# Kernel optimization log

Hardware: AMD Instinct MI355X
Metric: run time of the kernel (lower is better)

The kernel has to match this reference:

```python
import jax, jax.numpy as jnp
import numpy as np

ALPHA = 0.1
K = 5


def setup_inputs() -> dict:
    key = jax.random.key(0)
    ks = jax.random.split(key, 6)
    N, E = 50000, 800000
    IN, HID, OUT = 512, 256, 64
    x = jax.random.normal(ks[0], (N, IN), dtype=jnp.float32)
    edge_index = jax.random.randint(ks[1], (2, E), 0, N, dtype=jnp.int64)
    # Linear params (torch Linear: y = x @ W.T + b), kaiming-ish scale
    W1 = jax.random.normal(ks[2], (HID, IN), dtype=jnp.float32) / np.sqrt(IN)
    b1 = jnp.zeros((HID,), dtype=jnp.float32)
    W2 = jax.random.normal(ks[3], (OUT, HID), dtype=jnp.float32) / np.sqrt(HID)
    b2 = jnp.zeros((OUT,), dtype=jnp.float32)
    return {"x": x, "W1": W1, "b1": b1, "W2": W2, "b2": b2,
            "edge_index": edge_index}


def reference(x, W1, b1, W2, b2, edge_index):
    N = x.shape[0]
    # --- MLP encoder (eval mode: dropout is identity) ---
    h = jax.nn.relu(x @ W1.T + b1)          # [N, HID]
    h = h @ W2.T + b2                       # [N, OUT]

    # --- gcn_norm with self-loops (PyG APPNP default) ---
    src, dst = edge_index[0], edge_index[1]
    loop = jnp.arange(N, dtype=src.dtype)
    src_f = jnp.concatenate([src, loop])    # [E+N]
    dst_f = jnp.concatenate([dst, loop])
    ew = jnp.ones(src_f.shape[0], dtype=h.dtype)
    deg = jax.ops.segment_sum(ew, dst_f, num_segments=N)
    dinv = jnp.where(deg > 0, jax.lax.rsqrt(deg), 0.0)
    norm = dinv[src_f] * dinv[dst_f]        # [E+N]

    # --- K iterations of personalized-PageRank propagation ---
    def body(xk, _):
        msg = norm[:, None] * xk[src_f]                      # gather [E+N, OUT]
        agg = jax.ops.segment_sum(msg, dst_f, num_segments=N)
        return (1.0 - ALPHA) * agg + ALPHA * h, None

    xK, _ = jax.lax.scan(body, h, None, length=K)
    return jax.nn.log_softmax(xK, axis=1)
```

## Files before the change

kernel.cpp:

```cpp
#include <hip/hip_runtime.h>
#include <hip/hip_bf16.h>

#define IN_DIM  512
#define HID_DIM 256
#define OUT_DIM 64

typedef __attribute__((ext_vector_type(8))) short bf16x8;
typedef __attribute__((ext_vector_type(4))) float f32x4;

static __device__ __forceinline__ ushort f2b(float f) {
    __hip_bfloat16 b = __float2bfloat16(f);
    return *reinterpret_cast<ushort*>(&b);
}
static __device__ __forceinline__ float b2f_lo(uint u) {
    union { uint u; float f; } t; t.u = u << 16; return t.f;
}
static __device__ __forceinline__ float b2f_hi(uint u) {
    union { uint u; float f; } t; t.u = u & 0xFFFF0000u; return t.f;
}
static __device__ __forceinline__ uint packbf(float x, float y) {
    return (uint)f2b(x) | ((uint)f2b(y) << 16);
}

#define GLOAD16(g, l) __builtin_amdgcn_global_load_lds(                      \
    (const __attribute__((address_space(1))) void*)(g),                      \
    (__attribute__((address_space(3))) void*)(l), 16, 0, 0)


__global__ __launch_bounds__(256) void f2b_kernel(const float* __restrict__ in,
                                                  ushort* __restrict__ out, int n8) {
    for (int i = blockIdx.x * 256 + threadIdx.x; i < n8; i += gridDim.x * 256) {
        float4 a = *reinterpret_cast<const float4*>(&in[(size_t)i * 8]);
        float4 b = *reinterpret_cast<const float4*>(&in[(size_t)i * 8 + 4]);
        ushort4 lo = make_ushort4(f2b(a.x), f2b(a.y), f2b(a.z), f2b(a.w));
        ushort4 hi = make_ushort4(f2b(b.x), f2b(b.y), f2b(b.z), f2b(b.w));
        *reinterpret_cast<ushort4*>(&out[(size_t)i * 8])     = lo;
        *reinterpret_cast<ushort4*>(&out[(size_t)i * 8 + 4]) = hi;
    }
}


__global__ void hist_kernel(const int* __restrict__ ei, int* __restrict__ deg, int E) {
    int e = blockIdx.x * 256 + threadIdx.x;
    if (e < E) atomicAdd(&deg[ei[E + e]], 1);
}

__global__ __launch_bounds__(256) void scanA_kernel(const int* __restrict__ deg,
                                                    int* __restrict__ offs,
                                                    int* __restrict__ bsum, int N) {
    __shared__ int sh[256];
    int tid = threadIdx.x;
    int i = blockIdx.x * 256 + tid;
    int v = (i < N) ? deg[i] : 0;
    sh[tid] = v;
    __syncthreads();
#pragma unroll
    for (int off = 1; off < 256; off <<= 1) {
        int t = (tid >= off) ? sh[tid - off] : 0;
        __syncthreads();
        sh[tid] += t;
        __syncthreads();
    }
    if (i < N) offs[i] = sh[tid] - v;
    if (tid == 255) bsum[blockIdx.x] = sh[255];
}

__global__ __launch_bounds__(256) void scanB_kernel(int* __restrict__ bsum, int nb) {
    __shared__ int sh[256];
    int tid = threadIdx.x;
    int v = (tid < nb) ? bsum[tid] : 0;
    sh[tid] = v;
    __syncthreads();
#pragma unroll
    for (int off = 1; off < 256; off <<= 1) {
        int t = (tid >= off) ? sh[tid - off] : 0;
        __syncthreads();
        sh[tid] += t;
        __syncthreads();
    }
    if (tid < nb) bsum[tid] = sh[tid] - v;
}

__global__ __launch_bounds__(256) void scanC_kernel(const int* __restrict__ deg,
                                                    const int* __restrict__ bsum,
                                                    int* __restrict__ offs,
                                                    float* __restrict__ dinv,
                                                    int N, int E) {
    int i = blockIdx.x * 256 + threadIdx.x;
    if (i < N) {
        offs[i] += bsum[i >> 8];
        dinv[i] = rsqrtf((float)(deg[i] + 1));
    }
    if (i == 0) offs[N] = E;
}

__global__ void fill_kernel(const int* __restrict__ ei, const int* __restrict__ offs,
                            int* __restrict__ cursor, const float* __restrict__ dinv,
                            uint* __restrict__ edat, int E) {
    int e = blockIdx.x * 256 + threadIdx.x;
    if (e < E) {
        int s = ei[e];
        int d = ei[E + e];
        int pos = offs[d] + atomicAdd(&cursor[d], 1);
        edat[pos] = (uint)s | ((uint)f2b(dinv[d] * dinv[s]) << 16);
    }
}


__global__ __launch_bounds__(256) void gemm1_f32a(const float* __restrict__ A,
                                                  const ushort* __restrict__ B,
                                                  const float* __restrict__ bias,
                                                  ushort* __restrict__ C, int M) {
    constexpr int K = IN_DIM;
    constexpr int NK = K / 32;
    __shared__ float  Asf[2][128 * 32];
    __shared__ ushort Bs[2][128 * 32];

    const int tid  = threadIdx.x;
    const int lane = tid & 63;
    const int wid  = tid >> 6;
    const int wm = wid >> 1, wn = wid & 1;
    const int m0 = blockIdx.y * 128;
    const int n0 = blockIdx.x * 128;
    const int l15 = lane & 15;
    const int lq  = lane >> 4;

    const int a_row  = lane >> 3;
    const int a_slot = (lane & 7) ^ a_row;
    const int b_row  = lane >> 2;
    const int b_slot = (lane & 3) ^ ((lane >> 3) & 3);

    f32x4 acc[4][4];
#pragma unroll
    for (int i = 0; i < 4; ++i)
#pragma unroll
        for (int j = 0; j < 4; ++j) acc[i][j] = (f32x4)0.0f;

    auto stage = [&](int buf, int ks) {
        const int k0 = ks * 32;
#pragma unroll
        for (int q = 0; q < 4; ++q) {
            const int rbase = (wid * 4 + q) * 8;
            int am = m0 + rbase + a_row; if (am >= M) am = M - 1;
            const float* ga = A + (size_t)am * K + k0 + a_slot * 4;
            GLOAD16(ga, &Asf[buf][rbase * 32]);
        }
#pragma unroll
        for (int q = 0; q < 2; ++q) {
            const int rbase = (wid * 2 + q) * 16;
            const int row = rbase + b_row;
            const ushort* gb = B + (size_t)(n0 + row) * K + k0 + b_slot * 8;
            GLOAD16(gb, &Bs[buf][rbase * 32]);
        }
    };

    stage(0, 0);
    __syncthreads();

#pragma unroll 2
    for (int ks = 0; ks < NK; ++ks) {
        const int cur = ks & 1;
        if (ks + 1 < NK) stage(cur ^ 1, ks + 1);

        bf16x8 af[4], bf[4];
#pragma unroll
        for (int f = 0; f < 4; ++f) {
            const int ar = wm * 64 + f * 16 + l15;
            const int r7 = ar & 7;
            f32x4 v0 = *reinterpret_cast<const f32x4*>(&Asf[cur][ar * 32 + (((2 * lq) ^ r7) << 2)]);
            f32x4 v1 = *reinterpret_cast<const f32x4*>(&Asf[cur][ar * 32 + (((2 * lq + 1) ^ r7) << 2)]);
            bf16x8 a;
            a[0] = (short)f2b(v0[0]); a[1] = (short)f2b(v0[1]);
            a[2] = (short)f2b(v0[2]); a[3] = (short)f2b(v0[3]);
            a[4] = (short)f2b(v1[0]); a[5] = (short)f2b(v1[1]);
            a[6] = (short)f2b(v1[2]); a[7] = (short)f2b(v1[3]);
            af[f] = a;
            const int br = wn * 64 + f * 16 + l15;
            bf[f] = *reinterpret_cast<const bf16x8*>(&Bs[cur][br * 32 + ((lq ^ ((br >> 1) & 3)) << 3)]);
        }
#pragma unroll
        for (int i = 0; i < 4; ++i)
#pragma unroll
            for (int j = 0; j < 4; ++j)
                acc[i][j] = __builtin_amdgcn_mfma_f32_16x16x32_bf16(af[i], bf[j], acc[i][j], 0, 0, 0);

        __syncthreads();
    }

    const int lr = lq * 4;
#pragma unroll
    for (int nf = 0; nf < 4; ++nf) {
        int col = n0 + wn * 64 + nf * 16 + l15;
        float bv = bias[col];
#pragma unroll
        for (int mf = 0; mf < 4; ++mf) {
#pragma unroll
            for (int j = 0; j < 4; ++j) {
                int row = m0 + wm * 64 + mf * 16 + lr + j;
                if (row < M) {
                    float v = fmaxf(acc[mf][nf][j] + bv, 0.f);
                    C[(size_t)row * HID_DIM + col] = f2b(v);
                }
            }
        }
    }
}


#define LDT 40

__global__ __launch_bounds__(256) void gemm2_bf16(const ushort* __restrict__ A,
                                                  const float* __restrict__ B,
                                                  const float* __restrict__ bias,
                                                  ushort* __restrict__ Cb,
                                                  int M) {
    constexpr int K = HID_DIM;
    constexpr int NK = K / 32;
    __shared__ ushort As[128 * LDT];
    __shared__ ushort Bs[64 * LDT];

    const int tid = threadIdx.x;
    const int lane = tid & 63;
    const int wid = tid >> 6;
    const int wm = wid >> 1, wn = wid & 1;
    const int m0 = blockIdx.x * 128;
    const int l15 = lane & 15;
    const int koff = (lane >> 4) * 8;

    f32x4 acc[4][2];
#pragma unroll
    for (int i = 0; i < 4; ++i)
#pragma unroll
        for (int j = 0; j < 2; ++j) acc[i][j] = (f32x4)0.0f;

    uint4 rawA[2];
    float4 rbv[2];
#pragma unroll
    for (int i = 0; i < 2; ++i) {
        int slot = tid + i * 256;
        int rowA = slot >> 2, c8 = (slot & 3) << 3;
        int m = m0 + rowA;
        rawA[i] = (m < M) ? *reinterpret_cast<const uint4*>(&A[(size_t)m * K + c8])
                          : make_uint4(0u, 0u, 0u, 0u);
        int rowB = slot >> 3, c4 = (slot & 7) << 2;
        rbv[i] = *reinterpret_cast<const float4*>(&B[(size_t)rowB * K + c4]);
    }
#pragma unroll
    for (int i = 0; i < 2; ++i) {
        int slot = tid + i * 256;
        int rowA = slot >> 2, c8 = (slot & 3) << 3;
        *reinterpret_cast<uint4*>(&As[rowA * LDT + c8]) = rawA[i];
        int rowB = slot >> 3, c4 = (slot & 7) << 2;
        ushort4 ub = make_ushort4(f2b(rbv[i].x), f2b(rbv[i].y), f2b(rbv[i].z), f2b(rbv[i].w));
        *reinterpret_cast<ushort4*>(&Bs[rowB * LDT + c4]) = ub;
    }
    __syncthreads();

    for (int ks = 0; ks < NK; ++ks) {
        if (ks + 1 < NK) {
            int k0 = (ks + 1) * 32;
#pragma unroll
            for (int i = 0; i < 2; ++i) {
                int slot = tid + i * 256;
                int rowA = slot >> 2, c8 = (slot & 3) << 3;
                int m = m0 + rowA;
                rawA[i] = (m < M) ? *reinterpret_cast<const uint4*>(&A[(size_t)m * K + k0 + c8])
                                  : make_uint4(0u, 0u, 0u, 0u);
                int rowB = slot >> 3, c4 = (slot & 7) << 2;
                rbv[i] = *reinterpret_cast<const float4*>(&B[(size_t)rowB * K + k0 + c4]);
            }
        }
        bf16x8 af[4], bf[2];
#pragma unroll
        for (int f = 0; f < 4; ++f)
            af[f] = *reinterpret_cast<const bf16x8*>(&As[(wm * 64 + f * 16 + l15) * LDT + koff]);
#pragma unroll
        for (int f = 0; f < 2; ++f)
            bf[f] = *reinterpret_cast<const bf16x8*>(&Bs[(wn * 32 + f * 16 + l15) * LDT + koff]);
#pragma unroll
        for (int i = 0; i < 4; ++i)
#pragma unroll
            for (int j = 0; j < 2; ++j)
                acc[i][j] = __builtin_amdgcn_mfma_f32_16x16x32_bf16(af[i], bf[j], acc[i][j], 0, 0, 0);
        __syncthreads();
        if (ks + 1 < NK) {
#pragma unroll
            for (int i = 0; i < 2; ++i) {
                int slot = tid + i * 256;
                int rowA = slot >> 2, c8 = (slot & 3) << 3;
                *reinterpret_cast<uint4*>(&As[rowA * LDT + c8]) = rawA[i];
                int rowB = slot >> 3, c4 = (slot & 7) << 2;
                ushort4 ub = make_ushort4(f2b(rbv[i].x), f2b(rbv[i].y), f2b(rbv[i].z), f2b(rbv[i].w));
                *reinterpret_cast<ushort4*>(&Bs[rowB * LDT + c4]) = ub;
            }
            __syncthreads();
        }
    }

    const int lr = (lane >> 4) * 4;
#pragma unroll
    for (int nf = 0; nf < 2; ++nf) {
        int col = wn * 32 + nf * 16 + l15;
        float bv = bias[col];
#pragma unroll
        for (int mf = 0; mf < 4; ++mf) {
#pragma unroll
            for (int j = 0; j < 4; ++j) {
                int row = m0 + wm * 64 + mf * 16 + lr + j;
                if (row < M)
                    Cb[(size_t)row * OUT_DIM + col] = f2b(acc[mf][nf][j] + bv);
            }
        }
    }
}


__global__ __launch_bounds__(256) void propb_kernel(const uint* __restrict__ xin,
                                                    const uint* __restrict__ hb,
                                                    const float* __restrict__ dinv,
                                                    const int* __restrict__ offs,
                                                    const uint* __restrict__ edat,
                                                    uint* __restrict__ xout, int N) {
    int node = blockIdx.x * 8 + (threadIdx.x >> 5);
    int l32 = threadIdx.x & 31;
    if (node >= N) return;
    int e0 = offs[node], e1 = offs[node + 1];

    float ax[4] = {0.f, 0.f, 0.f, 0.f};
    float ay[4] = {0.f, 0.f, 0.f, 0.f};
    int e = e0;
    for (; e + 8 <= e1; e += 8) {
        uint p0 = edat[e+0], p1 = edat[e+1], p2 = edat[e+2], p3 = edat[e+3];
        uint p4 = edat[e+4], p5 = edat[e+5], p6 = edat[e+6], p7 = edat[e+7];
        uint g0 = xin[(size_t)(p0 & 0xFFFFu) * 32 + l32];
        uint g1 = xin[(size_t)(p1 & 0xFFFFu) * 32 + l32];
        uint g2 = xin[(size_t)(p2 & 0xFFFFu) * 32 + l32];
        uint g3 = xin[(size_t)(p3 & 0xFFFFu) * 32 + l32];
        uint g4 = xin[(size_t)(p4 & 0xFFFFu) * 32 + l32];
        uint g5 = xin[(size_t)(p5 & 0xFFFFu) * 32 + l32];
        uint g6 = xin[(size_t)(p6 & 0xFFFFu) * 32 + l32];
        uint g7 = xin[(size_t)(p7 & 0xFFFFu) * 32 + l32];
        ax[0] = fmaf(b2f_hi(p0), b2f_lo(g0), ax[0]); ay[0] = fmaf(b2f_hi(p0), b2f_hi(g0), ay[0]);
        ax[1] = fmaf(b2f_hi(p1), b2f_lo(g1), ax[1]); ay[1] = fmaf(b2f_hi(p1), b2f_hi(g1), ay[1]);
        ax[2] = fmaf(b2f_hi(p2), b2f_lo(g2), ax[2]); ay[2] = fmaf(b2f_hi(p2), b2f_hi(g2), ay[2]);
        ax[3] = fmaf(b2f_hi(p3), b2f_lo(g3), ax[3]); ay[3] = fmaf(b2f_hi(p3), b2f_hi(g3), ay[3]);
        ax[0] = fmaf(b2f_hi(p4), b2f_lo(g4), ax[0]); ay[0] = fmaf(b2f_hi(p4), b2f_hi(g4), ay[0]);
        ax[1] = fmaf(b2f_hi(p5), b2f_lo(g5), ax[1]); ay[1] = fmaf(b2f_hi(p5), b2f_hi(g5), ay[1]);
        ax[2] = fmaf(b2f_hi(p6), b2f_lo(g6), ax[2]); ay[2] = fmaf(b2f_hi(p6), b2f_hi(g6), ay[2]);
        ax[3] = fmaf(b2f_hi(p7), b2f_lo(g7), ax[3]); ay[3] = fmaf(b2f_hi(p7), b2f_hi(g7), ay[3]);
    }
    for (; e < e1; ++e) {
        uint p = edat[e];
        uint g = xin[(size_t)(p & 0xFFFFu) * 32 + l32];
        ax[0] = fmaf(b2f_hi(p), b2f_lo(g), ax[0]);
        ay[0] = fmaf(b2f_hi(p), b2f_hi(g), ay[0]);
    }
    float sx = (ax[0] + ax[1]) + (ax[2] + ax[3]);
    float sy = (ay[0] + ay[1]) + (ay[2] + ay[3]);
    float di = dinv[node];
    uint gs = xin[(size_t)node * 32 + l32];
    sx = fmaf(di * di, b2f_lo(gs), sx);
    sy = fmaf(di * di, b2f_hi(gs), sy);
    uint ah = hb[(size_t)node * 32 + l32];
    float r0 = 0.9f * sx + 0.1f * b2f_lo(ah);
    float r1 = 0.9f * sy + 0.1f * b2f_hi(ah);
    xout[(size_t)node * 32 + l32] = packbf(r0, r1);
}


__global__ __launch_bounds__(256) void propb_lsm_kernel(const uint* __restrict__ xin,
                                                        const uint* __restrict__ hb,
                                                        const float* __restrict__ dinv,
                                                        const int* __restrict__ offs,
                                                        const uint* __restrict__ edat,
                                                        float* __restrict__ out, int N) {
    int node = blockIdx.x * 8 + (threadIdx.x >> 5);
    int l32 = threadIdx.x & 31;
    if (node >= N) return;
    int e0 = offs[node], e1 = offs[node + 1];

    float ax[4] = {0.f, 0.f, 0.f, 0.f};
    float ay[4] = {0.f, 0.f, 0.f, 0.f};
    int e = e0;
    for (; e + 8 <= e1; e += 8) {
        uint p0 = edat[e+0], p1 = edat[e+1], p2 = edat[e+2], p3 = edat[e+3];
        uint p4 = edat[e+4], p5 = edat[e+5], p6 = edat[e+6], p7 = edat[e+7];
        uint g0 = xin[(size_t)(p0 & 0xFFFFu) * 32 + l32];
        uint g1 = xin[(size_t)(p1 & 0xFFFFu) * 32 + l32];
        uint g2 = xin[(size_t)(p2 & 0xFFFFu) * 32 + l32];
        uint g3 = xin[(size_t)(p3 & 0xFFFFu) * 32 + l32];
        uint g4 = xin[(size_t)(p4 & 0xFFFFu) * 32 + l32];
        uint g5 = xin[(size_t)(p5 & 0xFFFFu) * 32 + l32];
        uint g6 = xin[(size_t)(p6 & 0xFFFFu) * 32 + l32];
        uint g7 = xin[(size_t)(p7 & 0xFFFFu) * 32 + l32];
        ax[0] = fmaf(b2f_hi(p0), b2f_lo(g0), ax[0]); ay[0] = fmaf(b2f_hi(p0), b2f_hi(g0), ay[0]);
        ax[1] = fmaf(b2f_hi(p1), b2f_lo(g1), ax[1]); ay[1] = fmaf(b2f_hi(p1), b2f_hi(g1), ay[1]);
        ax[2] = fmaf(b2f_hi(p2), b2f_lo(g2), ax[2]); ay[2] = fmaf(b2f_hi(p2), b2f_hi(g2), ay[2]);
        ax[3] = fmaf(b2f_hi(p3), b2f_lo(g3), ax[3]); ay[3] = fmaf(b2f_hi(p3), b2f_hi(g3), ay[3]);
        ax[0] = fmaf(b2f_hi(p4), b2f_lo(g4), ax[0]); ay[0] = fmaf(b2f_hi(p4), b2f_hi(g4), ay[0]);
        ax[1] = fmaf(b2f_hi(p5), b2f_lo(g5), ax[1]); ay[1] = fmaf(b2f_hi(p5), b2f_hi(g5), ay[1]);
        ax[2] = fmaf(b2f_hi(p6), b2f_lo(g6), ax[2]); ay[2] = fmaf(b2f_hi(p6), b2f_hi(g6), ay[2]);
        ax[3] = fmaf(b2f_hi(p7), b2f_lo(g7), ax[3]); ay[3] = fmaf(b2f_hi(p7), b2f_hi(g7), ay[3]);
    }
    for (; e < e1; ++e) {
        uint p = edat[e];
        uint g = xin[(size_t)(p & 0xFFFFu) * 32 + l32];
        ax[0] = fmaf(b2f_hi(p), b2f_lo(g), ax[0]);
        ay[0] = fmaf(b2f_hi(p), b2f_hi(g), ay[0]);
    }
    float sx = (ax[0] + ax[1]) + (ax[2] + ax[3]);
    float sy = (ay[0] + ay[1]) + (ay[2] + ay[3]);
    float di = dinv[node];
    uint gs = xin[(size_t)node * 32 + l32];
    sx = fmaf(di * di, b2f_lo(gs), sx);
    sy = fmaf(di * di, b2f_hi(gs), sy);
    uint ah = hb[(size_t)node * 32 + l32];
    float r0 = 0.9f * sx + 0.1f * b2f_lo(ah);
    float r1 = 0.9f * sy + 0.1f * b2f_hi(ah);

    float m = fmaxf(r0, r1);
    for (int o = 16; o > 0; o >>= 1) m = fmaxf(m, __shfl_xor(m, o));
    float sum = expf(r0 - m) + expf(r1 - m);
    for (int o = 16; o > 0; o >>= 1) sum += __shfl_xor(sum, o);
    float ls = logf(sum);
    float2 o2 = make_float2(r0 - m - ls, r1 - m - ls);
    *reinterpret_cast<float2*>(&out[(size_t)node * 64 + l32 * 2]) = o2;
}


static inline size_t align256(size_t x) { return (x + 255) & ~(size_t)255; }

extern "C" void kernel_launch(void* const* d_in, const int* in_sizes, int n_in,
                              void* d_out, int out_size, void* d_ws, size_t ws_size,
                              hipStream_t stream) {
    const float* x  = (const float*)d_in[0];
    const float* W1 = (const float*)d_in[1];
    const float* b1 = (const float*)d_in[2];
    const float* W2 = (const float*)d_in[3];
    const float* b2 = (const float*)d_in[4];
    const int*   ei = (const int*)d_in[5];

    const int N = in_sizes[0] / IN_DIM;
    const int E = in_sizes[5] / 2;
    const int nb = (N + 255) / 256;

    char* base = (char*)d_ws;
    size_t off = 0;
    uint*  hb  = (uint*)(base + off);    off += align256((size_t)N * 32 * 4);
    uint*  xsa = (uint*)(base + off);    off += align256((size_t)N * 32 * 4);
    uint*  xsb = (uint*)(base + off);    off += align256((size_t)N * 32 * 4);
    ushort* w1b = (ushort*)(base + off); off += align256((size_t)HID_DIM * IN_DIM * 2);
    ushort* h1  = (ushort*)(base + off); off += align256((size_t)N * HID_DIM * 2);
    float* dinv = (float*)(base + off);  off += align256((size_t)N * 4);
    int*   deg  = (int*)(base + off);    off += align256((size_t)N * 4);
    int*   offs = (int*)(base + off);    off += align256((size_t)(N + 1) * 4);
    int*   cur  = (int*)(base + off);    off += align256((size_t)N * 4);
    int*   bsum = (int*)(base + off);    off += align256((size_t)nb * 4);
    uint*  edat = (uint*)(base + off);   off += align256((size_t)E * 4);

    hipMemsetAsync(deg, 0, (size_t)N * 4, stream);
    hipMemsetAsync(cur, 0, (size_t)N * 4, stream);
    hist_kernel<<<(E + 255) / 256, 256, 0, stream>>>(ei, deg, E);
    scanA_kernel<<<nb, 256, 0, stream>>>(deg, offs, bsum, N);
    scanB_kernel<<<1, 256, 0, stream>>>(bsum, nb);
    scanC_kernel<<<nb, 256, 0, stream>>>(deg, bsum, offs, dinv, N, E);
    fill_kernel<<<(E + 255) / 256, 256, 0, stream>>>(ei, offs, cur, dinv, edat, E);

    f2b_kernel<<<64, 256, 0, stream>>>(W1, w1b, HID_DIM * IN_DIM / 8);

    {
        dim3 g(HID_DIM / 128, (N + 127) / 128);
        gemm1_f32a<<<g, 256, 0, stream>>>(x, w1b, b1, h1, N);
    }
    {
        dim3 g((N + 127) / 128);
        gemm2_bf16<<<g, 256, 0, stream>>>(h1, W2, b2, (ushort*)hb, N);
    }

    int blocks = (N + 7) / 8;
    propb_kernel<<<blocks, 256, 0, stream>>>(hb,  hb, dinv, offs, edat, xsa, N);
    propb_kernel<<<blocks, 256, 0, stream>>>(xsa, hb, dinv, offs, edat, xsb, N);
    propb_kernel<<<blocks, 256, 0, stream>>>(xsb, hb, dinv, offs, edat, xsa, N);
    propb_kernel<<<blocks, 256, 0, stream>>>(xsa, hb, dinv, offs, edat, xsb, N);
    propb_lsm_kernel<<<blocks, 256, 0, stream>>>(xsb, hb, dinv, offs, edat,
                                                 (float*)d_out, N);
}
```

Before: 284.4 us.

## Keep W1 column slice resident in LDS and stream A directly to registers

Replaces the double-buffered LDS GEMM1 with a kernel that converts a 64-column slice of W1 to bf16 once into LDS (64 KB, swizzled). Each wave then streams its 32 rows of x straight from global memory into registers, with one-step register prefetch. This removes the separate W1 conversion kernel and the per-k-step barriers and LDS staging of A. In exchange, each block now re-reads and re-converts W1, A reuse across columns drops, and A loads are per-lane 32-byte strided rather than coalesced LDS-async copies.

Result: slower. 324.4 us (+14.1%).

```diff
diff --git a/kernel.cpp b/kernel.cpp
--- a/kernel.cpp
+++ b/kernel.cpp
@@ -20,23 +20,6 @@
 }
 static __device__ __forceinline__ uint packbf(float x, float y) {
     return (uint)f2b(x) | ((uint)f2b(y) << 16);
-}
-
-#define GLOAD16(g, l) __builtin_amdgcn_global_load_lds(                      \
-    (const __attribute__((address_space(1))) void*)(g),                      \
-    (__attribute__((address_space(3))) void*)(l), 16, 0, 0)
-
-
-__global__ __launch_bounds__(256) void f2b_kernel(const float* __restrict__ in,
-                                                  ushort* __restrict__ out, int n8) {
-    for (int i = blockIdx.x * 256 + threadIdx.x; i < n8; i += gridDim.x * 256) {
-        float4 a = *reinterpret_cast<const float4*>(&in[(size_t)i * 8]);
-        float4 b = *reinterpret_cast<const float4*>(&in[(size_t)i * 8 + 4]);
-        ushort4 lo = make_ushort4(f2b(a.x), f2b(a.y), f2b(a.z), f2b(a.w));
-        ushort4 hi = make_ushort4(f2b(b.x), f2b(b.y), f2b(b.z), f2b(b.w));
-        *reinterpret_cast<ushort4*>(&out[(size_t)i * 8])     = lo;
-        *reinterpret_cast<ushort4*>(&out[(size_t)i * 8 + 4]) = hi;
-    }
 }
 
 
@@ -107,98 +90,107 @@
 }
 
 
-__global__ __launch_bounds__(256) void gemm1_f32a(const float* __restrict__ A,
-                                                  const ushort* __restrict__ B,
-                                                  const float* __restrict__ bias,
-                                                  ushort* __restrict__ C, int M) {
+__global__ __launch_bounds__(512, 4) void gemm1_bres(const float* __restrict__ A,
+                                                     const float* __restrict__ W1,
+                                                     const float* __restrict__ bias,
+                                                     ushort* __restrict__ C, int M) {
     constexpr int K = IN_DIM;
     constexpr int NK = K / 32;
-    __shared__ float  Asf[2][128 * 32];
-    __shared__ ushort Bs[2][128 * 32];
+    __shared__ ushort Bs[64 * 512];
 
     const int tid  = threadIdx.x;
     const int lane = tid & 63;
-    const int wid  = tid >> 6;
-    const int wm = wid >> 1, wn = wid & 1;
-    const int m0 = blockIdx.y * 128;
-    const int n0 = blockIdx.x * 128;
+    const int w    = tid >> 6;
+    const int n0 = blockIdx.x * 64;
+    const int m0 = blockIdx.y * 256;
     const int l15 = lane & 15;
     const int lq  = lane >> 4;
 
-    const int a_row  = lane >> 3;
-    const int a_slot = (lane & 7) ^ a_row;
-    const int b_row  = lane >> 2;
-    const int b_slot = (lane & 3) ^ ((lane >> 3) & 3);
-
-    f32x4 acc[4][4];
-#pragma unroll
-    for (int i = 0; i < 4; ++i)
+    {
+        const int c = tid >> 3;
+        const int gb = (tid & 7) * 8;
+#pragma unroll
+        for (int i = 0; i < 8; ++i) {
+            const int g = gb + i;
+            const float* src = W1 + (size_t)(n0 + c) * K + g * 8;
+            float4 v0 = *reinterpret_cast<const float4*>(src);
+            float4 v1 = *reinterpret_cast<const float4*>(src + 4);
+            ushort4 u0 = make_ushort4(f2b(v0.x), f2b(v0.y), f2b(v0.z), f2b(v0.w));
+            ushort4 u1 = make_ushort4(f2b(v1.x), f2b(v1.y), f2b(v1.z), f2b(v1.w));
+            ushort* dst = &Bs[c * 512 + (g ^ (c & 7)) * 8];
+            *reinterpret_cast<ushort4*>(dst)     = u0;
+            *reinterpret_cast<ushort4*>(dst + 4) = u1;
+        }
+    }
+    __syncthreads();
+
+    const int r0 = m0 + w * 32;
+    const int koff = lq * 8;
+
+    int arow0 = r0 + l15;      if (arow0 >= M) arow0 = M - 1;
+    int arow1 = r0 + 16 + l15; if (arow1 >= M) arow1 = M - 1;
+    const float* ga0 = A + (size_t)arow0 * K + koff;
+    const float* ga1 = A + (size_t)arow1 * K + koff;
+
+    f32x4 acc[2][4];
+#pragma unroll
+    for (int i = 0; i < 2; ++i)
 #pragma unroll
         for (int j = 0; j < 4; ++j) acc[i][j] = (f32x4)0.0f;
 
-    auto stage = [&](int buf, int ks) {
-        const int k0 = ks * 32;
-#pragma unroll
-        for (int q = 0; q < 4; ++q) {
-            const int rbase = (wid * 4 + q) * 8;
-            int am = m0 + rbase + a_row; if (am >= M) am = M - 1;
-            const float* ga = A + (size_t)am * K + k0 + a_slot * 4;
-            GLOAD16(ga, &Asf[buf][rbase * 32]);
-        }
-#pragma unroll
-        for (int q = 0; q < 2; ++q) {
-            const int rbase = (wid * 2 + q) * 16;
-            const int row = rbase + b_row;
-            const ushort* gb = B + (size_t)(n0 + row) * K + k0 + b_slot * 8;
-            GLOAD16(gb, &Bs[buf][rbase * 32]);
-        }
-    };
-
-    stage(0, 0);
-    __syncthreads();
-
-#pragma unroll 2
+    float4 pv[2][2];
+    pv[0][0] = *reinterpret_cast<const float4*>(ga0);
+    pv[0][1] = *reinterpret_cast<const float4*>(ga0 + 4);
+    pv[1][0] = *reinterpret_cast<const float4*>(ga1);
+    pv[1][1] = *reinterpret_cast<const float4*>(ga1 + 4);
+
     for (int ks = 0; ks < NK; ++ks) {
-        const int cur = ks & 1;
-        if (ks + 1 < NK) stage(cur ^ 1, ks + 1);
-
-        bf16x8 af[4], bf[4];
-#pragma unroll
-        for (int f = 0; f < 4; ++f) {
-            const int ar = wm * 64 + f * 16 + l15;
-            const int r7 = ar & 7;
-            f32x4 v0 = *reinterpret_cast<const f32x4*>(&Asf[cur][ar * 32 + (((2 * lq) ^ r7) << 2)]);
-            f32x4 v1 = *reinterpret_cast<const f32x4*>(&Asf[cur][ar * 32 + (((2 * lq + 1) ^ r7) << 2)]);
+        float4 cv[2][2];
+#pragma unroll
+        for (int rf = 0; rf < 2; ++rf) { cv[rf][0] = pv[rf][0]; cv[rf][1] = pv[rf][1]; }
+        if (ks + 1 < NK) {
+            const int k1 = (ks + 1) * 32;
+            pv[0][0] = *reinterpret_cast<const float4*>(ga0 + k1);
+            pv[0][1] = *reinterpret_cast<const float4*>(ga0 + k1 + 4);
+            pv[1][0] = *reinterpret_cast<const float4*>(ga1 + k1);
+            pv[1][1] = *reinterpret_cast<const float4*>(ga1 + k1 + 4);
+        }
+        bf16x8 af[2];
+#pragma unroll
+        for (int rf = 0; rf < 2; ++rf) {
             bf16x8 a;
-            a[0] = (short)f2b(v0[0]); a[1] = (short)f2b(v0[1]);
-            a[2] = (short)f2b(v0[2]); a[3] = (short)f2b(v0[3]);
-            a[4] = (short)f2b(v1[0]); a[5] = (short)f2b(v1[1]);
-            a[6] = (short)f2b(v1[2]); a[7] = (short)f2b(v1[3]);
-            af[f] = a;
-            const int br = wn * 64 + f * 16 + l15;
-            bf[f] = *reinterpret_cast<const bf16x8*>(&Bs[cur][br * 32 + ((lq ^ ((br >> 1) & 3)) << 3)]);
-        }
-#pragma unroll
-        for (int i = 0; i < 4; ++i)
-#pragma unroll
-            for (int j = 0; j < 4; ++j)
-                acc[i][j] = __builtin_amdgcn_mfma_f32_16x16x32_bf16(af[i], bf[j], acc[i][j], 0, 0, 0);
-
-        __syncthreads();
+            a[0] = (short)f2b(cv[rf][0].x); a[1] = (short)f2b(cv[rf][0].y);
+            a[2] = (short)f2b(cv[rf][0].z); a[3] = (short)f2b(cv[rf][0].w);
+            a[4] = (short)f2b(cv[rf][1].x); a[5] = (short)f2b(cv[rf][1].y);
+            a[6] = (short)f2b(cv[rf][1].z); a[7] = (short)f2b(cv[rf][1].w);
+            af[rf] = a;
+        }
+        bf16x8 bf[4];
+#pragma unroll
+        for (int cf = 0; cf < 4; ++cf) {
+            const int c = cf * 16 + l15;
+            const int g = ks * 4 + lq;
+            bf[cf] = *reinterpret_cast<const bf16x8*>(&Bs[c * 512 + (g ^ (c & 7)) * 8]);
+        }
+#pragma unroll
+        for (int rf = 0; rf < 2; ++rf)
+#pragma unroll
+            for (int cf = 0; cf < 4; ++cf)
+                acc[rf][cf] = __builtin_amdgcn_mfma_f32_16x16x32_bf16(af[rf], bf[cf], acc[rf][cf], 0, 0, 0);
     }
 
     const int lr = lq * 4;
 #pragma unroll
-    for (int nf = 0; nf < 4; ++nf) {
-        int col = n0 + wn * 64 + nf * 16 + l15;
+    for (int cf = 0; cf < 4; ++cf) {
+        int col = n0 + cf * 16 + l15;
         float bv = bias[col];
 #pragma unroll
-        for (int mf = 0; mf < 4; ++mf) {
+        for (int rf = 0; rf < 2; ++rf) {
 #pragma unroll
             for (int j = 0; j < 4; ++j) {
-                int row = m0 + wm * 64 + mf * 16 + lr + j;
+                int row = r0 + rf * 16 + lr + j;
                 if (row < M) {
-                    float v = fmaxf(acc[mf][nf][j] + bv, 0.f);
+                    float v = fmaxf(acc[rf][cf][j] + bv, 0.f);
                     C[(size_t)row * HID_DIM + col] = f2b(v);
                 }
             }
@@ -449,7 +441,6 @@
     uint*  hb  = (uint*)(base + off);    off += align256((size_t)N * 32 * 4);
     uint*  xsa = (uint*)(base + off);    off += align256((size_t)N * 32 * 4);
     uint*  xsb = (uint*)(base + off);    off += align256((size_t)N * 32 * 4);
-    ushort* w1b = (ushort*)(base + off); off += align256((size_t)HID_DIM * IN_DIM * 2);
     ushort* h1  = (ushort*)(base + off); off += align256((size_t)N * HID_DIM * 2);
     float* dinv = (float*)(base + off);  off += align256((size_t)N * 4);
     int*   deg  = (int*)(base + off);    off += align256((size_t)N * 4);
@@ -466,11 +457,9 @@
     scanC_kernel<<<nb, 256, 0, stream>>>(deg, bsum, offs, dinv, N, E);
     fill_kernel<<<(E + 255) / 256, 256, 0, stream>>>(ei, offs, cur, dinv, edat, E);
 
-    f2b_kernel<<<64, 256, 0, stream>>>(W1, w1b, HID_DIM * IN_DIM / 8);
-
     {
-        dim3 g(HID_DIM / 128, (N + 127) / 128);
-        gemm1_f32a<<<g, 256, 0, stream>>>(x, w1b, b1, h1, N);
+        dim3 g(4, (N + 255) / 256);
+        gemm1_bres<<<g, 512, 0, stream>>>(x, W1, b1, h1, N);
     }
     {
         dim3 g((N + 127) / 128);
```
